# Performance work log

Measured on AMD Instinct MI355X. Metric: run time of the kernel, lower is better.

The kernel has to match this reference:

```python
import jax, jax.numpy as jnp
import numpy as np

B = 256          # number of enclosing subgraphs (one candidate link each)
N_PER = 128      # nodes per subgraph (== max_nodes)
N = B * N_PER
DEG = 8
E_REAL = N * DEG
E = E_REAL + 2 * B
H = 32           # hidden_channels
HEADS = 2
WALK_LEN = 7
MAX_Z = 1000
L = 3            # num_layers
LRELU = 0.2


def setup_inputs() -> dict:
    rng = np.random.default_rng(0)
    goff = (np.arange(B) * N_PER)[:, None]
    # real edges: random sources, tiled targets so every node has >=1 incoming edge
    lr = rng.integers(0, N_PER, size=(B, N_PER * DEG))
    lc = np.broadcast_to(np.tile(np.arange(N_PER), DEG), (B, N_PER * DEG))
    row_real = (lr + goff).reshape(-1)
    col_real = (lc + goff).reshape(-1)
    # one candidate link (i,j) per graph, stored as interleaved (i->j, j->i)
    i_loc = rng.integers(0, N_PER, size=B)
    j_loc = (i_loc + 1 + rng.integers(0, N_PER - 1, size=B)) % N_PER
    node_i = i_loc + np.arange(B) * N_PER
    node_j = j_loc + np.arange(B) * N_PER
    cand_row = np.stack([node_i, node_j], 1).reshape(-1)
    cand_col = np.stack([node_j, node_i], 1).reshape(-1)
    key = jax.random.key(0)
    ks = jax.random.split(key, 10)
    s = 0.05
    return dict(
        z_table=jax.random.normal(ks[1], (MAX_Z, H)) * s,
        conv_W=jax.random.normal(ks[2], (L, H, H)) * s,
        conv_b=jnp.zeros((L, H)),
        k1_W=jax.random.normal(ks[3], (H, H)) * s, k1_b=jnp.zeros((H,)),
        q1_W=jax.random.normal(ks[4], (H, H)) * s, q1_b=jnp.zeros((H,)),
        k2_W=jax.random.normal(ks[5], (H, HEADS * H)) * s, k2_b=jnp.zeros((HEADS * H,)),
        q2_W=jax.random.normal(ks[6], (H, HEADS * H)) * s, q2_b=jnp.zeros((HEADS * H,)),
        mlp_W1=jax.random.normal(ks[7], (WALK_LEN * HEADS * 5 + HEADS, H)) * s,
        mlp_b1=jnp.zeros((H,)),
        mlp_W2=jax.random.normal(ks[8], (H, 1)) * s,
        mlp_b2=jnp.zeros((1,)),
        z=jax.random.randint(ks[0], (N,), 0, MAX_Z, dtype=jnp.int32),
        edge_row=jnp.asarray(np.concatenate([row_real, cand_row]), jnp.int32),
        edge_col=jnp.asarray(np.concatenate([col_real, cand_col]), jnp.int32),
        edge_mask=jnp.asarray(np.concatenate([np.ones(E_REAL, bool), np.zeros(2 * B, bool)])),
        batch=jnp.repeat(jnp.arange(B, dtype=jnp.int32), N_PER),
        node_i=jnp.asarray(node_i, jnp.int32),
        node_j=jnp.asarray(node_j, jnp.int32),
    )


def _forward(z_table, conv_W, conv_b, k1_W, k1_b, q1_W, q1_b, k2_W, k2_b, q2_W, q2_b,
             mlp_W1, mlp_b1, mlp_W2, mlp_b2,
             z, edge_row, edge_col, edge_mask, batch, node_i, node_j):
    # ---- GCN stack (eval mode: dropout / dropedge are identity) ----
    x = z_table[z]                                    # (N, H)
    loops = jnp.arange(N, dtype=edge_row.dtype)
    row2 = jnp.concatenate([edge_row, loops])         # add self loops
    col2 = jnp.concatenate([edge_col, loops])
    deg = jax.ops.segment_sum(jnp.ones_like(col2, x.dtype), col2, N)
    dinv = jax.lax.rsqrt(deg)                         # deg >= 1 due to self loops
    gnorm = dinv[row2] * dinv[col2]
    for l in range(L):
        xw = x @ conv_W[l]
        x = jax.ops.segment_sum(gnorm[:, None] * xw[row2], col2, N) + conv_b[l]
        if l < L - 1:
            x = jax.nn.relu(x)
    # ---- WalkPooling attention weights ----
    q = jax.nn.leaky_relu(x @ k1_W + k1_b, LRELU)
    k = jax.nn.leaky_relu(x @ q1_W + q1_b, LRELU)
    q = (q @ k2_W + k2_b).reshape(N, HEADS, H)
    k = (k @ q2_W + q2_b).reshape(N, HEADS, H)
    w = jnp.sum(q[edge_row] * k[edge_col], -1) / np.sqrt(H)   # (E, HEADS)
    wmax = jax.ops.segment_max(w, edge_col, N)
    ew = jnp.exp(w - wmax[edge_col])
    weights_p = ew / (jax.ops.segment_sum(ew, edge_col, N)[edge_col] + 1e-16)
    ewm = ew * edge_mask[:, None]                     # candidate link removed
    weights_m = ewm / (jax.ops.segment_sum(ewm, edge_col, N)[edge_col] + 1e-16)
    # omega: scores at the 2B candidate edges (stored last), summed per pair
    wc = jax.nn.sigmoid(w[E_REAL:])                   # (2B, HEADS)
    omega = wc[1::2] + wc[0::2]                       # (B, HEADS)
    # local node index within each graph
    arangeN = jnp.arange(N, dtype=jnp.int32)
    starts = jax.ops.segment_min(arangeN, batch, B)
    index = arangeN - starts[batch]                   # (N,)
    idx_i = index[node_i]
    idx_j = index[node_j]
    x0 = jnp.zeros((N, N_PER), x.dtype).at[arangeN, index].set(1.0)
    x0 = jnp.broadcast_to(x0, (HEADS, N, N_PER))

    def propagate(xh, wcol):                          # xh (HEADS,N,M), wcol (E,HEADS)
        def one(xi, wi):
            return jax.ops.segment_sum(wi[:, None] * xi[edge_row], edge_col, N)
        return jax.vmap(one, in_axes=(0, 1))(xh, wcol)

    xp = propagate(x0, weights_p)
    xm = propagate(x0, weights_m)

    def feats(xh):
        nl = xh[:, node_i, idx_i] + xh[:, node_j, idx_j]   # (HEADS, B)
        ll = xh[:, node_i, idx_j] + xh[:, node_j, idx_i]
        diag = xh[:, arangeN, index]                        # (HEADS, N)
        g = jax.vmap(lambda d: jax.ops.segment_sum(d, batch, B))(diag)
        return nl, ll, g

    def step(carry, _):
        xp, xm = carry
        xp = propagate(xp, weights_p)
        xm = propagate(xm, weights_m)
        nlp, llp, gp = feats(xp)
        nlm, llm, gm = feats(xm)
        return (xp, xm), (nlp, nlm, llp, llm, gp - gm)

    _, (nlp, nlm, llp, llm, gl) = jax.lax.scan(step, (xp, xm), None, length=WALK_LEN)

    def to_feat(a):                                    # (WALK_LEN,HEADS,B) -> (B, HEADS*WALK_LEN)
        return jnp.transpose(a, (2, 1, 0)).reshape(B, HEADS * WALK_LEN)

    feat = jnp.concatenate([to_feat(gl), omega, to_feat(nlp), to_feat(nlm),
                            to_feat(llp), to_feat(llm)], axis=1)   # (B, 72)
    h1 = jax.nn.relu(feat @ mlp_W1 + mlp_b1)
    return h1 @ mlp_W2 + mlp_b2                        # (B, 1)


def reference(z_table, conv_W, conv_b, k1_W, k1_b, q1_W, q1_b, k2_W, k2_b, q2_W, q2_b,
              mlp_W1, mlp_b1, mlp_W2, mlp_b2,
              z, edge_row, edge_col, edge_mask, batch, node_i, node_j):
    return _forward(z_table, conv_W, conv_b, k1_W, k1_b, q1_W, q1_b, k2_W, k2_b,
                    q2_W, q2_b, mlp_W1, mlp_b1, mlp_W2, mlp_b2,
                    z, edge_row, edge_col, edge_mask, batch, node_i, node_j)
```

## Files before the change

kernel.cpp:

```cpp
#include <hip/hip_runtime.h>

#define NB 256
#define NPER 128
#define NN 32768
#define DEG 8
#define EREAL (NN*DEG)
#define HH 32
#define NHEADS 2
#define WLEN 7
#define RSQRT_H 0.17677669529663687f

#define FRONT_LDS 136208
#define WALK_LDS  40960

__global__ __launch_bounds__(1024) void k_front(
    const float* __restrict__ z_table, const int* __restrict__ z,
    const float* __restrict__ convW, const float* __restrict__ convb,
    const float* __restrict__ k1W, const float* __restrict__ k1b,
    const float* __restrict__ q1W, const float* __restrict__ q1b,
    const float* __restrict__ k2W, const float* __restrict__ k2b,
    const float* __restrict__ q2W, const float* __restrict__ q2b,
    const int* __restrict__ erow, const int* __restrict__ node_i, const int* __restrict__ node_j,
    float2* __restrict__ wp8, float* __restrict__ rat_g,
    float* __restrict__ exw_g, float* __restrict__ omega_g)
{
    extern __shared__ char sm[];
    float* xl   = (float*)sm;
    float* t1   = (float*)(sm + 16384);
    float* t2   = (float*)(sm + 32768);
    float* Wb   = (float*)(sm + 49152);
    float* rowf = (float*)(sm + 65536);
    float* colf = (float*)(sm + 98304);
    int*   rows = (int*)(sm + 131072);
    float* dinv = (float*)(sm + 135168);
    float* bias = (float*)(sm + 135680);
    float* omg  = (float*)(sm + 136192);

    int b = blockIdx.x, tid = threadIdx.x;
    int iloc = node_i[b] & 127, jloc = node_j[b] & 127;

    #pragma unroll
    for (int ii=0;ii<4;ii++){
        int i = tid + ii*1024;
        int n = i>>5, d = i&31;
        xl[i] = z_table[z[b*128+n]*32 + d];
    }
    rows[(tid&127)*8 + (tid>>7)] = erow[b*1024 + tid] & 127;
    if (tid < 128) dinv[tid] = rsqrtf((tid==iloc||tid==jloc)? 10.f : 9.f);

    int j = tid & 31, rg = tid>>5;
    for (int l=0;l<3;l++){
        __syncthreads();
        Wb[tid] = convW[l*1024+tid];
        if (tid<32) bias[tid] = convb[l*32+tid];
        __syncthreads();
        float Wc[32];
        #pragma unroll
        for (int k=0;k<32;k++) Wc[k] = Wb[k*32+j];
        #pragma unroll
        for (int ii=0;ii<4;ii++){
            int r = rg + 32*ii;
            const float4* xr = (const float4*)&xl[r*32];
            float a = 0.f;
            #pragma unroll
            for (int k4=0;k4<8;k4++){
                float4 xv = xr[k4];
                a += xv.x*Wc[4*k4] + xv.y*Wc[4*k4+1] + xv.z*Wc[4*k4+2] + xv.w*Wc[4*k4+3];
            }
            t1[r*32+j] = a;
        }
        __syncthreads();
        #pragma unroll
        for (int ii=0;ii<4;ii++){
            int c = rg + 32*ii;
            float acc = dinv[c]*t1[c*32+j];
            #pragma unroll
            for (int s=0;s<8;s++){
                int r = rows[c*8+s];
                acc += dinv[r]*t1[r*32+j];
            }
            if (c==iloc) acc += dinv[jloc]*t1[jloc*32+j];
            if (c==jloc) acc += dinv[iloc]*t1[iloc*32+j];
            float v = dinv[c]*acc + bias[j];
            if (l<2) v = fmaxf(v,0.f);
            xl[c*32+j] = v;
        }
    }
    __syncthreads();
    for (int i=tid;i<2048;i+=1024) Wb[i] = (i<1024)? k1W[i] : q1W[i-1024];
    if (tid<64) bias[tid] = (tid<32)? k1b[tid] : q1b[tid-32];
    __syncthreads();
    {
        float Wa[32], Wq[32];
        #pragma unroll
        for (int k=0;k<32;k++){ Wa[k] = Wb[k*32+j]; Wq[k] = Wb[1024 + k*32+j]; }
        #pragma unroll
        for (int ii=0;ii<4;ii++){
            int n = rg + 32*ii;
            const float4* xr = (const float4*)&xl[n*32];
            float a1 = bias[j], a2 = bias[32+j];
            #pragma unroll
            for (int k4=0;k4<8;k4++){
                float4 xv = xr[k4];
                a1 += xv.x*Wa[4*k4] + xv.y*Wa[4*k4+1] + xv.z*Wa[4*k4+2] + xv.w*Wa[4*k4+3];
                a2 += xv.x*Wq[4*k4] + xv.y*Wq[4*k4+1] + xv.z*Wq[4*k4+2] + xv.w*Wq[4*k4+3];
            }
            t1[n*32+j] = a1>0.f? a1 : 0.2f*a1;
            t2[n*32+j] = a2>0.f? a2 : 0.2f*a2;
        }
    }
    __syncthreads();
    for (int i=tid;i<4096;i+=1024) Wb[i] = (i<2048)? k2W[i] : q2W[i-2048];
    if (tid<128) bias[tid] = (tid<64)? k2b[tid] : q2b[tid-64];
    __syncthreads();
    {
        int j2 = tid & 63, rg2 = tid>>6;
        float Wk[32], Wq[32];
        #pragma unroll
        for (int k=0;k<32;k++){ Wk[k] = Wb[k*64+j2]; Wq[k] = Wb[2048 + k*64+j2]; }
        #pragma unroll
        for (int ii=0;ii<8;ii++){
            int n = rg2 + 16*ii;
            const float4* u4 = (const float4*)&t1[n*32];
            const float4* v4 = (const float4*)&t2[n*32];
            float o1 = bias[j2], o2 = bias[64+j2];
            #pragma unroll
            for (int k4=0;k4<8;k4++){
                float4 u = u4[k4], v = v4[k4];
                o1 += u.x*Wk[4*k4] + u.y*Wk[4*k4+1] + u.z*Wk[4*k4+2] + u.w*Wk[4*k4+3];
                o2 += v.x*Wq[4*k4] + v.y*Wq[4*k4+1] + v.z*Wq[4*k4+2] + v.w*Wq[4*k4+3];
            }
            int sidx = n*64 + ((((j2>>2) ^ (n&7)) << 2) | (j2&3));
            rowf[sidx] = o1;
            colf[sidx] = o2;
        }
    }
    float* warr = Wb;
    __syncthreads();
    {
        int c = tid & 127, h = (tid>>7)&1, sgrp = tid>>8;
        int cs = c&7, h8 = h*8;
        const float4* cf = (const float4*)&colf[c*64];
        float4 kv[8];
        #pragma unroll
        for (int k4=0;k4<8;k4++) kv[k4] = cf[h8 + (k4^cs)];
        #pragma unroll
        for (int si=0;si<2;si++){
            int s = sgrp*2+si;
            int r = rows[c*8+s];
            int rs = r&7;
            const float4* rf = (const float4*)&rowf[r*64];
            float a = 0.f;
            #pragma unroll
            for (int k4=0;k4<8;k4++){
                float4 q = rf[h8 + (k4^rs)];
                a += q.x*kv[k4].x + q.y*kv[k4].y + q.z*kv[k4].z + q.w*kv[k4].w;
            }
            warr[(h*128+c)*9+s] = a*RSQRT_H;
        }
        if (sgrp==0){
            int r = -1;
            if (c==jloc) r = iloc; else if (c==iloc) r = jloc;
            float a = -3.0e38f;
            if (r>=0){
                int rs = r&7;
                const float4* rf = (const float4*)&rowf[r*64];
                a = 0.f;
                #pragma unroll
                for (int k4=0;k4<8;k4++){
                    float4 q = rf[h8 + (k4^rs)];
                    a += q.x*kv[k4].x + q.y*kv[k4].y + q.z*kv[k4].z + q.w*kv[k4].w;
                }
                a *= RSQRT_H;
            }
            warr[(h*128+c)*9+8] = a;
        }
    }
    __syncthreads();
    if (tid < 256){
        int c = tid & 127, h = tid >> 7;
        float wv[9];
        #pragma unroll
        for (int s=0;s<9;s++) wv[s] = warr[(h*128+c)*9+s];
        float wmax = wv[0];
        #pragma unroll
        for (int s=1;s<9;s++) wmax = fmaxf(wmax, wv[s]);
        float e[9]; float sp = 0.f;
        #pragma unroll
        for (int s=0;s<9;s++){ e[s] = expf(wv[s]-wmax); sp += e[s]; }
        float sm_ = sp - e[8];
        float rp = 1.f/(sp+1e-16f);
        float rat = (sp+1e-16f)/(sm_+1e-16f);
        size_t base = ((size_t)h*NN + b*128 + c)*8;
        #pragma unroll
        for (int s=0;s<8;s++)
            wp8[base+s] = make_float2(e[s]*rp, __int_as_float(rows[c*8+s]<<8));
        rat_g[h*NN + b*128 + c] = rat;
        if (c==jloc || c==iloc){
            int k = (c==jloc)? 0 : 1;
            exw_g[(b*2+h)*2 + k] = e[8]*rp;
            omg[h*2+k] = 1.f/(1.f+expf(-wv[8]));
        }
    }
    __syncthreads();
    if (tid < 2) omega_g[b*2+tid] = omg[tid*2] + omg[tid*2+1];
}

__global__ __launch_bounds__(512, 8) void k_walk(
    const float2* __restrict__ wp8, const float* __restrict__ rat_g,
    const float* __restrict__ exw_g,
    const int* __restrict__ node_i, const int* __restrict__ node_j,
    float* __restrict__ featbuf)
{
    extern __shared__ char sm[];
    float* A = (float*)sm;
    float2* wr = (float2*)(sm + 32768);
    int bid = blockIdx.x;
    int b = bid>>3, h = (bid>>2)&1, sg = (bid>>1)&1, vh = bid&1;
    int vbase = vh*64;
    int tid = threadIdx.x, lane = tid&63, wid = tid>>6;
    int qg = lane>>4, l16 = lane&15;

    for (int i=tid;i<1024;i+=512){
        float2 p = wp8[((size_t)h*NN + b*128)*8 + i];
        if (sg) p.x *= rat_g[h*NN + b*128 + (i>>3)];
        wr[i] = p;
    }
    int iloc = node_i[b]&127, jloc = node_j[b]&127;
    float exw0=0.f, exw1=0.f; int exc0=-1, exc1=-1;
    if (!sg){
        exw0 = exw_g[(b*2+h)*2+0];
        exw1 = exw_g[(b*2+h)*2+1];
        exc0 = jloc; exc1 = iloc;
    }
    int exo0 = iloc<<8, exo1 = jloc<<8;
    for (int i=tid;i<8192;i+=512) A[i] = 0.f;
    __syncthreads();
    if (tid < 128){
        int c = tid;
        #pragma unroll
        for (int s=0;s<8;s++){
            float2 p = wr[c*8+s];
            int vl = (__float_as_int(p.y)>>8) - vbase;
            if ((unsigned)vl < 64u) A[c*64+vl] += p.x;
        }
        if (c==exc0){ int vl=(exo0>>8)-vbase; if((unsigned)vl<64u) A[c*64+vl]+=exw0; }
        if (c==exc1){ int vl=(exo1>>8)-vbase; if((unsigned)vl<64u) A[c*64+vl]+=exw1; }
    }
    __syncthreads();
    int vb4 = l16<<4;
    float4 accs[4];
    for (int t=0;t<WLEN;t++){
        #pragma unroll
        for (int pi=0;pi<4;pi++){
            int c = (wid<<4) + (pi<<2) + qg;
            float4 a = {0.f,0.f,0.f,0.f};
            #pragma unroll
            for (int s=0;s<8;s++){
                float2 p = wr[c*8+s];
                const float4 v = *(const float4*)(sm + __float_as_int(p.y) + vb4);
                a.x += p.x*v.x; a.y += p.x*v.y; a.z += p.x*v.z; a.w += p.x*v.w;
            }
            if (c==exc0){ const float4 v=*(const float4*)(sm+exo0+vb4);
                a.x+=exw0*v.x; a.y+=exw0*v.y; a.z+=exw0*v.z; a.w+=exw0*v.w; }
            if (c==exc1){ const float4 v=*(const float4*)(sm+exo1+vb4);
                a.x+=exw1*v.x; a.y+=exw1*v.y; a.z+=exw1*v.z; a.w+=exw1*v.w; }
            accs[pi] = a;
        }
        __syncthreads();
        #pragma unroll
        for (int pi=0;pi<4;pi++){
            int c = (wid<<4) + (pi<<2) + qg;
            *(float4*)&A[c*64 + (l16<<2)] = accs[pi];
        }
        __syncthreads();
        if (wid==0){
            float ts = A[(vbase+lane)*64 + lane];
            #pragma unroll
            for (int off=32;off;off>>=1) ts += __shfl_down(ts, off);
            if (lane==0) featbuf[(((2*2+sg)*WLEN + t)*(NHEADS*NB) + h*NB + b)*2 + vh] = ts;
        } else if (wid==1 && lane==0){
            float nl=0.f, ll=0.f;
            int vi = iloc - vbase, vj = jloc - vbase;
            if ((unsigned)vi<64u){ nl += A[iloc*64+vi]; ll += A[jloc*64+vi]; }
            if ((unsigned)vj<64u){ nl += A[jloc*64+vj]; ll += A[iloc*64+vj]; }
            featbuf[(((0*2+sg)*WLEN + t)*(NHEADS*NB) + h*NB + b)*2 + vh] = nl;
            featbuf[(((1*2+sg)*WLEN + t)*(NHEADS*NB) + h*NB + b)*2 + vh] = ll;
        }
    }
}

__global__ __launch_bounds__(256) void k_final(const float* __restrict__ W1, const float* __restrict__ b1,
                       const float* __restrict__ W2, const float* __restrict__ b2,
                       const float* __restrict__ featbuf, const float* __restrict__ omega,
                       float* __restrict__ out){
    __shared__ float sW1[72*HH];
    __shared__ float sb1[HH];
    __shared__ float sW2[HH];
    __shared__ float sb2;
    int tid = threadIdx.x;
    for (int i=tid;i<72*HH;i+=256) sW1[i] = W1[i];
    if (tid<HH){ sb1[tid]=b1[tid]; sW2[tid]=W2[tid]; }
    if (tid==0) sb2 = b2[0];
    __syncthreads();
    int b = tid;
    float h1[HH];
    #pragma unroll
    for (int j2=0;j2<HH;j2++) h1[j2] = sb1[j2];
    auto rd = [&](int idx){ return featbuf[idx*2] + featbuf[idx*2+1]; };
    auto addf = [&](int fi, float v){
        #pragma unroll
        for (int j2=0;j2<HH;j2++) h1[j2] += v * sW1[fi*HH + j2];
    };
    for (int h2=0;h2<NHEADS;h2++)
        for (int t=0;t<WLEN;t++){
            float gp = rd(((2*2+0)*WLEN+t)*(NHEADS*NB)+h2*NB+b);
            float gm = rd(((2*2+1)*WLEN+t)*(NHEADS*NB)+h2*NB+b);
            addf(h2*WLEN+t, gp-gm);
        }
    for (int h2=0;h2<NHEADS;h2++) addf(14+h2, omega[b*NHEADS+h2]);
    for (int h2=0;h2<NHEADS;h2++)
        for (int t=0;t<WLEN;t++){
            addf(16+h2*WLEN+t, rd(((0*2+0)*WLEN+t)*(NHEADS*NB)+h2*NB+b));
            addf(30+h2*WLEN+t, rd(((0*2+1)*WLEN+t)*(NHEADS*NB)+h2*NB+b));
            addf(44+h2*WLEN+t, rd(((1*2+0)*WLEN+t)*(NHEADS*NB)+h2*NB+b));
            addf(58+h2*WLEN+t, rd(((1*2+1)*WLEN+t)*(NHEADS*NB)+h2*NB+b));
        }
    float o = sb2;
    #pragma unroll
    for (int j2=0;j2<HH;j2++) o += fmaxf(h1[j2],0.f)*sW2[j2];
    out[b] = o;
}

extern "C" void kernel_launch(void* const* d_in, const int* in_sizes, int n_in,
                              void* d_out, int out_size, void* d_ws, size_t ws_size,
                              hipStream_t stream){
    const float* z_table = (const float*)d_in[0];
    const float* convW   = (const float*)d_in[1];
    const float* convb   = (const float*)d_in[2];
    const float* k1W     = (const float*)d_in[3];
    const float* k1b     = (const float*)d_in[4];
    const float* q1W     = (const float*)d_in[5];
    const float* q1b     = (const float*)d_in[6];
    const float* k2W     = (const float*)d_in[7];
    const float* k2b     = (const float*)d_in[8];
    const float* q2W     = (const float*)d_in[9];
    const float* q2b     = (const float*)d_in[10];
    const float* mW1     = (const float*)d_in[11];
    const float* mb1     = (const float*)d_in[12];
    const float* mW2     = (const float*)d_in[13];
    const float* mb2     = (const float*)d_in[14];
    const int* z         = (const int*)d_in[15];
    const int* erow      = (const int*)d_in[16];
    const int* node_i    = (const int*)d_in[20];
    const int* node_j    = (const int*)d_in[21];
    float* out = (float*)d_out;

    char* ws = (char*)d_ws;
    size_t off = 0;
    auto alloc = [&](size_t bytes){ void* p = ws + off; off += (bytes + 255) & ~255ULL; return p; };
    float2* wp8     = (float2*)alloc((size_t)NHEADS*NN*8*8);
    float*  rat     = (float*) alloc((size_t)NHEADS*NN*4);
    float*  exw     = (float*) alloc((size_t)NB*NHEADS*2*4);
    float*  omega   = (float*) alloc((size_t)NB*NHEADS*4);
    float*  featbuf = (float*) alloc((size_t)3*2*WLEN*NHEADS*NB*2*4);

    hipFuncSetAttribute((const void*)k_front, hipFuncAttributeMaxDynamicSharedMemorySize, FRONT_LDS);
    hipFuncSetAttribute((const void*)k_walk,  hipFuncAttributeMaxDynamicSharedMemorySize, WALK_LDS);

    k_front<<<NB,   1024, FRONT_LDS, stream>>>(z_table, z, convW, convb,
                                               k1W,k1b,q1W,q1b,k2W,k2b,q2W,q2b,
                                               erow, node_i, node_j, wp8, rat, exw, omega);
    k_walk <<<NB*8, 512,  WALK_LDS,  stream>>>(wp8, rat, exw, node_i, node_j, featbuf);
    k_final<<<1,    256,  0,         stream>>>(mW1, mb1, mW2, mb2, featbuf, omega, out);
}
```

Before: 214.9 us.

## Compute walk traces via matrix powers and vector-walk for node/link features

Rewrites the random-walk kernel to build the full 128x128 propagation matrix per block and compute P^2..P^4 with three sparse multiplies. The traces of higher powers up to P^8 come from Frobenius-style inner products of those powers instead of seven successive full propagations. Node and link landing probabilities are tracked with a separate 64-lane vector walk using shuffles, and an XOR swizzle is added to the LDS layout to avoid bank conflicts. Blocks go from 512 to 1024 threads with a larger LDS footprint, which lowers occupancy, and the reordered sums may shift floating-point rounding.

After: 230.8 us. +7.4%, slower.

```diff
diff --git a/kernel.cpp b/kernel.cpp
--- a/kernel.cpp
+++ b/kernel.cpp
@@ -11,7 +11,11 @@
 #define RSQRT_H 0.17677669529663687f
 
 #define FRONT_LDS 136208
-#define WALK_LDS  40960
+#define WALK2_LDS 140544
+
+__device__ __forceinline__ int sidx8(int n, int v){
+    return n*128 + ((((v>>2) ^ (n&31))<<2) | (v&3));
+}
 
 __global__ __launch_bounds__(1024) void k_front(
     const float* __restrict__ z_table, const int* __restrict__ z,
@@ -194,7 +198,7 @@
         size_t base = ((size_t)h*NN + b*128 + c)*8;
         #pragma unroll
         for (int s=0;s<8;s++)
-            wp8[base+s] = make_float2(e[s]*rp, __int_as_float(rows[c*8+s]<<8));
+            wp8[base+s] = make_float2(e[s]*rp, __int_as_float(rows[c*8+s]));
         rat_g[h*NN + b*128 + c] = rat;
         if (c==jloc || c==iloc){
             int k = (c==jloc)? 0 : 1;
@@ -206,25 +210,24 @@
     if (tid < 2) omega_g[b*2+tid] = omg[tid*2] + omg[tid*2+1];
 }
 
-__global__ __launch_bounds__(512, 8) void k_walk(
+__global__ __launch_bounds__(1024, 4) void k_walk(
     const float2* __restrict__ wp8, const float* __restrict__ rat_g,
     const float* __restrict__ exw_g,
     const int* __restrict__ node_i, const int* __restrict__ node_j,
     float* __restrict__ featbuf)
 {
     extern __shared__ char sm[];
-    float* A = (float*)sm;
-    float2* wr = (float2*)(sm + 32768);
+    float*  PX = (float*)sm;
+    float*  PY = (float*)(sm + 65536);
+    float2* wr = (float2*)(sm + 131072);
+    float*  scr= (float*)(sm + 140288);
     int bid = blockIdx.x;
-    int b = bid>>3, h = (bid>>2)&1, sg = (bid>>1)&1, vh = bid&1;
-    int vbase = vh*64;
-    int tid = threadIdx.x, lane = tid&63, wid = tid>>6;
-    int qg = lane>>4, l16 = lane&15;
-
-    for (int i=tid;i<1024;i+=512){
-        float2 p = wp8[((size_t)h*NN + b*128)*8 + i];
-        if (sg) p.x *= rat_g[h*NN + b*128 + (i>>3)];
-        wr[i] = p;
+    int b = bid>>2, h = (bid>>1)&1, sg = bid&1;
+    int tid = threadIdx.x;
+
+    {   float2 p = wp8[((size_t)h*NN + b*128)*8 + tid];
+        if (sg) p.x *= rat_g[h*NN + b*128 + (tid>>3)];
+        wr[tid] = p;
     }
     int iloc = node_i[b]&127, jloc = node_j[b]&127;
     float exw0=0.f, exw1=0.f; int exc0=-1, exc1=-1;
@@ -233,60 +236,171 @@
         exw1 = exw_g[(b*2+h)*2+1];
         exc0 = jloc; exc1 = iloc;
     }
-    int exo0 = iloc<<8, exo1 = jloc<<8;
-    for (int i=tid;i<8192;i+=512) A[i] = 0.f;
+    {   float4* PX4 = (float4*)PX;
+        #pragma unroll
+        for (int k=0;k<4;k++) PX4[tid + k*1024] = make_float4(0.f,0.f,0.f,0.f);
+    }
     __syncthreads();
     if (tid < 128){
         int c = tid;
         #pragma unroll
         for (int s=0;s<8;s++){
             float2 p = wr[c*8+s];
-            int vl = (__float_as_int(p.y)>>8) - vbase;
-            if ((unsigned)vl < 64u) A[c*64+vl] += p.x;
-        }
-        if (c==exc0){ int vl=(exo0>>8)-vbase; if((unsigned)vl<64u) A[c*64+vl]+=exw0; }
-        if (c==exc1){ int vl=(exo1>>8)-vbase; if((unsigned)vl<64u) A[c*64+vl]+=exw1; }
-    }
-    __syncthreads();
-    int vb4 = l16<<4;
-    float4 accs[4];
-    for (int t=0;t<WLEN;t++){
-        #pragma unroll
-        for (int pi=0;pi<4;pi++){
-            int c = (wid<<4) + (pi<<2) + qg;
-            float4 a = {0.f,0.f,0.f,0.f};
-            #pragma unroll
-            for (int s=0;s<8;s++){
-                float2 p = wr[c*8+s];
-                const float4 v = *(const float4*)(sm + __float_as_int(p.y) + vb4);
-                a.x += p.x*v.x; a.y += p.x*v.y; a.z += p.x*v.z; a.w += p.x*v.w;
-            }
-            if (c==exc0){ const float4 v=*(const float4*)(sm+exo0+vb4);
-                a.x+=exw0*v.x; a.y+=exw0*v.y; a.z+=exw0*v.z; a.w+=exw0*v.w; }
-            if (c==exc1){ const float4 v=*(const float4*)(sm+exo1+vb4);
-                a.x+=exw1*v.x; a.y+=exw1*v.y; a.z+=exw1*v.z; a.w+=exw1*v.w; }
-            accs[pi] = a;
-        }
-        __syncthreads();
-        #pragma unroll
-        for (int pi=0;pi<4;pi++){
-            int c = (wid<<4) + (pi<<2) + qg;
-            *(float4*)&A[c*64 + (l16<<2)] = accs[pi];
-        }
-        __syncthreads();
-        if (wid==0){
-            float ts = A[(vbase+lane)*64 + lane];
-            #pragma unroll
-            for (int off=32;off;off>>=1) ts += __shfl_down(ts, off);
-            if (lane==0) featbuf[(((2*2+sg)*WLEN + t)*(NHEADS*NB) + h*NB + b)*2 + vh] = ts;
-        } else if (wid==1 && lane==0){
-            float nl=0.f, ll=0.f;
-            int vi = iloc - vbase, vj = jloc - vbase;
-            if ((unsigned)vi<64u){ nl += A[iloc*64+vi]; ll += A[jloc*64+vi]; }
-            if ((unsigned)vj<64u){ nl += A[jloc*64+vj]; ll += A[iloc*64+vj]; }
-            featbuf[(((0*2+sg)*WLEN + t)*(NHEADS*NB) + h*NB + b)*2 + vh] = nl;
-            featbuf[(((1*2+sg)*WLEN + t)*(NHEADS*NB) + h*NB + b)*2 + vh] = ll;
-        }
+            PX[sidx8(c, __float_as_int(p.y))] += p.x;
+        }
+        if (c==exc0) PX[sidx8(c, iloc)] += exw0;
+        if (c==exc1) PX[sidx8(c, jloc)] += exw1;
+    }
+    if (tid < 64){
+        int l = tid;
+        float ci0 = (iloc==l)?1.f:0.f, ci1 = (iloc==64+l)?1.f:0.f;
+        float cj0 = (jloc==l)?1.f:0.f, cj1 = (jloc==64+l)?1.f:0.f;
+        int il = iloc&63, jl = jloc&63;
+        for (int t=1;t<=9;t++){
+            float a0 = __shfl(ci0, il), a1 = __shfl(ci1, il);
+            float b0 = __shfl(cj0, il), b1 = __shfl(cj1, il);
+            float c0 = __shfl(ci0, jl), c1 = __shfl(ci1, jl);
+            float d0 = __shfl(cj0, jl), d1 = __shfl(cj1, jl);
+            float vi_ci = (iloc<64)? a0:a1;
+            float vi_cj = (iloc<64)? b0:b1;
+            float vj_ci = (jloc<64)? c0:c1;
+            float vj_cj = (jloc<64)? d0:d1;
+            if (t>=3 && l==0){
+                int tt = t-3;
+                featbuf[((0*2+sg)*WLEN + tt)*(NHEADS*NB) + h*NB + b] = vi_ci + vj_cj;
+                featbuf[((1*2+sg)*WLEN + tt)*(NHEADS*NB) + h*NB + b] = vi_cj + vj_ci;
+            }
+            if (t<=8){
+                float nci0=0.f,ncj0=0.f,nci1=0.f,ncj1=0.f;
+                #pragma unroll
+                for (int s=0;s<8;s++){
+                    float2 p0 = wr[l*8+s];
+                    int r0 = __float_as_int(p0.y);
+                    float xlo = __shfl(ci0, r0&63), xhi = __shfl(ci1, r0&63);
+                    float ylo = __shfl(cj0, r0&63), yhi = __shfl(cj1, r0&63);
+                    nci0 += p0.x * ((r0<64)? xlo:xhi);
+                    ncj0 += p0.x * ((r0<64)? ylo:yhi);
+                    float2 p1 = wr[(64+l)*8+s];
+                    int r1 = __float_as_int(p1.y);
+                    xlo = __shfl(ci0, r1&63); xhi = __shfl(ci1, r1&63);
+                    ylo = __shfl(cj0, r1&63); yhi = __shfl(cj1, r1&63);
+                    nci1 += p1.x * ((r1<64)? xlo:xhi);
+                    ncj1 += p1.x * ((r1<64)? ylo:yhi);
+                }
+                if (exc0==l)    { nci0 += exw0*vi_ci; ncj0 += exw0*vi_cj; }
+                if (exc0==64+l) { nci1 += exw0*vi_ci; ncj1 += exw0*vi_cj; }
+                if (exc1==l)    { nci0 += exw1*vj_ci; ncj0 += exw1*vj_cj; }
+                if (exc1==64+l) { nci1 += exw1*vj_ci; ncj1 += exw1*vj_cj; }
+                ci0=nci0; ci1=nci1; cj0=ncj0; cj1=ncj1;
+            }
+        }
+    }
+    __syncthreads();
+
+    int c = tid>>3, q0 = (tid&7)<<2, cx = c&31;
+    auto mult = [&](float* dst, const float* src){
+        float4 a0={0,0,0,0}, a1={0,0,0,0}, a2={0,0,0,0}, a3={0,0,0,0};
+        #pragma unroll
+        for (int s=0;s<8;s++){
+            float2 p = wr[c*8+s];
+            int r = __float_as_int(p.y);
+            const float4* srow = (const float4*)src + r*32;
+            int rx = r&31;
+            float4 v0=srow[(q0+0)^rx], v1=srow[(q0+1)^rx], v2=srow[(q0+2)^rx], v3=srow[(q0+3)^rx];
+            a0.x+=p.x*v0.x; a0.y+=p.x*v0.y; a0.z+=p.x*v0.z; a0.w+=p.x*v0.w;
+            a1.x+=p.x*v1.x; a1.y+=p.x*v1.y; a1.z+=p.x*v1.z; a1.w+=p.x*v1.w;
+            a2.x+=p.x*v2.x; a2.y+=p.x*v2.y; a2.z+=p.x*v2.z; a2.w+=p.x*v2.w;
+            a3.x+=p.x*v3.x; a3.y+=p.x*v3.y; a3.z+=p.x*v3.z; a3.w+=p.x*v3.w;
+        }
+        if (c==exc0){
+            const float4* srow = (const float4*)src + iloc*32; int rx = iloc&31;
+            float4 v0=srow[(q0+0)^rx], v1=srow[(q0+1)^rx], v2=srow[(q0+2)^rx], v3=srow[(q0+3)^rx];
+            a0.x+=exw0*v0.x; a0.y+=exw0*v0.y; a0.z+=exw0*v0.z; a0.w+=exw0*v0.w;
+            a1.x+=exw0*v1.x; a1.y+=exw0*v1.y; a1.z+=exw0*v1.z; a1.w+=exw0*v1.w;
+            a2.x+=exw0*v2.x; a2.y+=exw0*v2.y; a2.z+=exw0*v2.z; a2.w+=exw0*v2.w;
+            a3.x+=exw0*v3.x; a3.y+=exw0*v3.y; a3.z+=exw0*v3.z; a3.w+=exw0*v3.w;
+        }
+        if (c==exc1){
+            const float4* srow = (const float4*)src + jloc*32; int rx = jloc&31;
+            float4 v0=srow[(q0+0)^rx], v1=srow[(q0+1)^rx], v2=srow[(q0+2)^rx], v3=srow[(q0+3)^rx];
+            a0.x+=exw1*v0.x; a0.y+=exw1*v0.y; a0.z+=exw1*v0.z; a0.w+=exw1*v0.w;
+            a1.x+=exw1*v1.x; a1.y+=exw1*v1.y; a1.z+=exw1*v1.z; a1.w+=exw1*v1.w;
+            a2.x+=exw1*v2.x; a2.y+=exw1*v2.y; a2.z+=exw1*v2.z; a2.w+=exw1*v2.w;
+            a3.x+=exw1*v3.x; a3.y+=exw1*v3.y; a3.z+=exw1*v3.z; a3.w+=exw1*v3.w;
+        }
+        float4* drow = (float4*)dst + c*32;
+        drow[(q0+0)^cx]=a0; drow[(q0+1)^cx]=a1; drow[(q0+2)^cx]=a2; drow[(q0+3)^cx]=a3;
+    };
+    auto wreduce = [](float v){
+        #pragma unroll
+        for (int o=32;o;o>>=1) v += __shfl_down(v,o);
+        return v;
+    };
+
+    mult(PY, PX);
+    __syncthreads();
+    mult(PX, PY);
+    if (tid<128){
+        float d = wreduce(PY[sidx8(tid,tid)]);
+        if ((tid&63)==0) scr[0+(tid>>6)] = d;
+    }
+    __syncthreads();
+    mult(PY, PX);
+    if (tid<128){
+        float d = wreduce(PX[sidx8(tid,tid)]);
+        if ((tid&63)==0) scr[2+(tid>>6)] = d;
+    }
+    __syncthreads();
+    if (tid<128){
+        float d = wreduce(PY[sidx8(tid,tid)]);
+        if ((tid&63)==0) scr[4+(tid>>6)] = d;
+        float s5 = 0.f;
+        #pragma unroll
+        for (int s=0;s<8;s++){
+            float2 p = wr[tid*8+s];
+            s5 += p.x * PY[sidx8(__float_as_int(p.y), tid)];
+        }
+        if (tid==exc0) s5 += exw0 * PY[sidx8(iloc, jloc)];
+        if (tid==exc1) s5 += exw1 * PY[sidx8(jloc, iloc)];
+        s5 = wreduce(s5);
+        if ((tid&63)==0) scr[6+(tid>>6)] = s5;
+    }
+    {
+        int a = c, ax = cx;
+        const float4* x3 = (const float4*)PX + a*32;
+        const float4* x4 = (const float4*)PY + a*32;
+        float t6=0.f, t7=0.f, t8=0.f;
+        #pragma unroll
+        for (int k=0;k<4;k++){
+            int q = q0+k;
+            float4 a3 = x3[q^ax], a4 = x4[q^ax];
+            #pragma unroll
+            for (int e=0;e<4;e++){
+                int bb = q*4+e;
+                int bi = sidx8(bb, a);
+                float b3 = PX[bi], b4 = PY[bi];
+                float a3e = ((float*)&a3)[e], a4e = ((float*)&a4)[e];
+                t6 += a3e*b3; t7 += a3e*b4; t8 += a4e*b4;
+            }
+        }
+        t6 = wreduce(t6); t7 = wreduce(t7); t8 = wreduce(t8);
+        int w = tid>>6;
+        if ((tid&63)==0){ scr[8+w]=t6; scr[24+w]=t7; scr[40+w]=t8; }
+    }
+    __syncthreads();
+    if (tid==0){
+        float tr2=scr[0]+scr[1], tr3=scr[2]+scr[3], tr4=scr[4]+scr[5], tr5=scr[6]+scr[7];
+        float t6=0.f,t7=0.f,t8=0.f;
+        #pragma unroll
+        for (int w=0;w<16;w++){ t6+=scr[8+w]; t7+=scr[24+w]; t8+=scr[40+w]; }
+        int gb = ((2*2+sg)*WLEN)*(NHEADS*NB) + h*NB + b;
+        featbuf[gb+0*(NHEADS*NB)] = tr2;
+        featbuf[gb+1*(NHEADS*NB)] = tr3;
+        featbuf[gb+2*(NHEADS*NB)] = tr4;
+        featbuf[gb+3*(NHEADS*NB)] = tr5;
+        featbuf[gb+4*(NHEADS*NB)] = t6;
+        featbuf[gb+5*(NHEADS*NB)] = t7;
+        featbuf[gb+6*(NHEADS*NB)] = t8;
     }
 }
 
@@ -307,7 +421,7 @@
     float h1[HH];
     #pragma unroll
     for (int j2=0;j2<HH;j2++) h1[j2] = sb1[j2];
-    auto rd = [&](int idx){ return featbuf[idx*2] + featbuf[idx*2+1]; };
+    auto rd = [&](int idx){ return featbuf[idx]; };
     auto addf = [&](int fi, float v){
         #pragma unroll
         for (int j2=0;j2<HH;j2++) h1[j2] += v * sW1[fi*HH + j2];
@@ -363,14 +477,14 @@
     float*  rat     = (float*) alloc((size_t)NHEADS*NN*4);
     float*  exw     = (float*) alloc((size_t)NB*NHEADS*2*4);
     float*  omega   = (float*) alloc((size_t)NB*NHEADS*4);
-    float*  featbuf = (float*) alloc((size_t)3*2*WLEN*NHEADS*NB*2*4);
+    float*  featbuf = (float*) alloc((size_t)3*2*WLEN*NHEADS*NB*4);
 
     hipFuncSetAttribute((const void*)k_front, hipFuncAttributeMaxDynamicSharedMemorySize, FRONT_LDS);
-    hipFuncSetAttribute((const void*)k_walk,  hipFuncAttributeMaxDynamicSharedMemorySize, WALK_LDS);
+    hipFuncSetAttribute((const void*)k_walk,  hipFuncAttributeMaxDynamicSharedMemorySize, WALK2_LDS);
 
     k_front<<<NB,   1024, FRONT_LDS, stream>>>(z_table, z, convW, convb,
                                                k1W,k1b,q1W,q1b,k2W,k2b,q2W,q2b,
                                                erow, node_i, node_j, wp8, rat, exw, omega);
-    k_walk <<<NB*8, 512,  WALK_LDS,  stream>>>(wp8, rat, exw, node_i, node_j, featbuf);
+    k_walk <<<NB*4, 1024, WALK2_LDS, stream>>>(wp8, rat, exw, node_i, node_j, featbuf);
     k_final<<<1,    256,  0,         stream>>>(mW1, mb1, mW2, mb2, featbuf, omega, out);
 }
```
